# Kernel tuning notes

Hardware: AMD Instinct MI355X
Metric: run time of the kernel (lower is better)

Reference implementation:

```python
import jax, jax.numpy as jnp
import numpy as np

GROUPS = 8
EPS = 1e-5


def group_norm_dim1(x, gamma, beta):
    # Faithful to torch: GroupNorm treats dim 1 (height) as the channel axis.
    B, H, W, C = x.shape
    xg = x.reshape(B, GROUPS, H // GROUPS, W, C)
    mean = xg.mean(axis=(2, 3, 4), keepdims=True)
    var = xg.var(axis=(2, 3, 4), keepdims=True)
    xn = ((xg - mean) * jax.lax.rsqrt(var + EPS)).reshape(B, H, W, C)
    return xn * gamma[None, :, None, None] + beta[None, :, None, None]


def setup_inputs() -> dict:
    key = jax.random.key(0)
    ks = jax.random.split(key, 8)
    B, H, W, C = 4, 64, 64, 64  # height must equal units for GroupNorm to apply
    s = 1.0 / np.sqrt(C)
    return {
        "x": jax.random.normal(ks[0], (B, H, W, C), dtype=jnp.float32),
        "gamma": jnp.ones((C,), jnp.float32),
        "beta": jnp.zeros((C,), jnp.float32),
        "Wq": jax.random.normal(ks[1], (C, C), jnp.float32) * s,
        "bq": jnp.zeros((C,), jnp.float32),
        "Wk": jax.random.normal(ks[2], (C, C), jnp.float32) * s,
        "bk": jnp.zeros((C,), jnp.float32),
        "Wv": jax.random.normal(ks[3], (C, C), jnp.float32) * s,
        "bv": jnp.zeros((C,), jnp.float32),
        "Wo": jax.random.normal(ks[4], (C, C), jnp.float32) * s,
        "bo": jnp.zeros((C,), jnp.float32),
    }


def reference(x, gamma, beta, Wq, bq, Wk, bk, Wv, bv, Wo, bo):
    B, H, W, C = x.shape
    scale = C ** (-0.5)
    xn = group_norm_dim1(x, gamma, beta)
    q = xn @ Wq + bq
    k = xn @ Wk + bk
    v = xn @ Wv + bv
    # full spatial self-attention: scores [B, H, W, H*W]
    scores = jnp.einsum('bhwc,bijc->bhwij', q, k) * scale
    attn = jax.nn.softmax(scores.reshape(B, H, W, H * W), axis=-1)
    attn = attn.reshape(B, H, W, H, W)
    proj = jnp.einsum('bhwij,bijc->bhwc', attn, v)
    proj = proj @ Wo + bo
    return xn + proj
```

## Files before the change

### kernel.cpp

```cpp
#include <hip/hip_runtime.h>

typedef __bf16 bf16_t;
typedef bf16_t bf16x8 __attribute__((ext_vector_type(8)));
typedef bf16_t bf16x4 __attribute__((ext_vector_type(4)));
typedef float  f32x4  __attribute__((ext_vector_type(4)));

#define MFMA32(a, b, c) __builtin_amdgcn_mfma_f32_16x16x32_bf16(a, b, c, 0, 0, 0)

typedef __attribute__((address_space(3))) unsigned int       lds_u32;
typedef __attribute__((address_space(1))) const unsigned int glb_u32c;
#define DMA16(GP, LP) __builtin_amdgcn_global_load_lds((glb_u32c*)(const void*)(GP), \
                                                       (lds_u32*)(void*)(LP), 16, 0, 0)

__global__ __launch_bounds__(256) void gn1w_kernel(const float* __restrict__ x,
    float2* __restrict__ partials,
    const float* __restrict__ Wq, const float* __restrict__ Wk,
    const float* __restrict__ Wv, const float* __restrict__ Wo,
    bf16_t* __restrict__ Wt) {
  int blk = blockIdx.x, t = threadIdx.x;
  if (blk >= 256) {
    int idx = (blk - 256) * 256 + t;
    int wsel = idx >> 12, rem = idx & 4095;
    int c = rem >> 6, kk = rem & 63;
    const float* src = (wsel == 0) ? Wq : ((wsel == 1) ? Wk : ((wsel == 2) ? Wv : Wo));
    Wt[idx] = (bf16_t)src[kk * 64 + c];
    return;
  }
  const float4* x4 = (const float4*)x + (size_t)blk * 1024;
  float s = 0.f, sq = 0.f;
  #pragma unroll
  for (int u = 0; u < 4; ++u) {
    float4 v = x4[u * 256 + t];
    s  += v.x + v.y + v.z + v.w;
    sq += v.x * v.x + v.y * v.y + v.z * v.z + v.w * v.w;
  }
  for (int off = 32; off; off >>= 1) {
    s  += __shfl_down(s, off, 64);
    sq += __shfl_down(sq, off, 64);
  }
  __shared__ float2 ps[4];
  if ((t & 63) == 0) ps[t >> 6] = make_float2(s, sq);
  __syncthreads();
  if (t == 0) {
    float S = 0.f, Q = 0.f;
    #pragma unroll
    for (int i = 0; i < 4; ++i) { S += ps[i].x; Q += ps[i].y; }
    partials[blk] = make_float2(S, Q);
  }
}

__global__ __launch_bounds__(256) void gnqkv_kernel(
    const float* __restrict__ x, const float* __restrict__ gamma,
    const float* __restrict__ beta, const float2* __restrict__ parts,
    const bf16_t* __restrict__ Wt,
    const float* __restrict__ bq, const float* __restrict__ bk, const float* __restrict__ bv,
    bf16_t* __restrict__ xnb, bf16_t* __restrict__ qo, bf16_t* __restrict__ ko,
    bf16_t* __restrict__ vo) {
  __shared__ __align__(16) bf16_t xl[4096];
  int blk = blockIdx.x, t = threadIdx.x;
  int grp = blk >> 3;
  float S = 0.f, Q = 0.f;
  #pragma unroll
  for (int i = 0; i < 8; ++i) { float2 p = parts[grp * 8 + i]; S += p.x; Q += p.y; }
  float mean = S * (1.f / 32768.f);
  float rstd = rsqrtf(Q * (1.f / 32768.f) - mean * mean + 1e-5f);
  int h = blk & 63;
  float ga = gamma[h] * rstd;
  float be = beta[h] - mean * ga;
  {
    int r = t >> 2, col0 = (t & 3) * 16;
    const float4* x4 = (const float4*)(x + (size_t)blk * 4096 + r * 64 + col0);
    bf16x8 pk0, pk1;
    float4 v0 = x4[0], v1 = x4[1], v2 = x4[2], v3 = x4[3];
    pk0[0] = (bf16_t)(v0.x * ga + be); pk0[1] = (bf16_t)(v0.y * ga + be);
    pk0[2] = (bf16_t)(v0.z * ga + be); pk0[3] = (bf16_t)(v0.w * ga + be);
    pk0[4] = (bf16_t)(v1.x * ga + be); pk0[5] = (bf16_t)(v1.y * ga + be);
    pk0[6] = (bf16_t)(v1.z * ga + be); pk0[7] = (bf16_t)(v1.w * ga + be);
    pk1[0] = (bf16_t)(v2.x * ga + be); pk1[1] = (bf16_t)(v2.y * ga + be);
    pk1[2] = (bf16_t)(v2.z * ga + be); pk1[3] = (bf16_t)(v2.w * ga + be);
    pk1[4] = (bf16_t)(v3.x * ga + be); pk1[5] = (bf16_t)(v3.y * ga + be);
    pk1[6] = (bf16_t)(v3.z * ga + be); pk1[7] = (bf16_t)(v3.w * ga + be);
    *(bf16x8*)&xnb[(size_t)blk * 4096 + r * 64 + col0]     = pk0;
    *(bf16x8*)&xnb[(size_t)blk * 4096 + r * 64 + col0 + 8] = pk1;
    int sw = r & 7, j0 = (t & 3) * 2;
    *(bf16x8*)&xl[r * 64 + ((j0 ^ sw) << 3)]       = pk0;
    *(bf16x8*)&xl[r * 64 + (((j0 + 1) ^ sw) << 3)] = pk1;
  }
  __syncthreads();
  int w = t >> 6, lane = t & 63, quad = lane >> 4, l16 = lane & 15;
  int rl = w * 16 + l16, sw2 = rl & 7;
  bf16x8 a0 = *(const bf16x8*)&xl[rl * 64 + ((quad ^ sw2) << 3)];
  bf16x8 a1 = *(const bf16x8*)&xl[rl * 64 + (((quad + 4) ^ sw2) << 3)];
  int m0 = blk * 64 + w * 16;
  int bi = blk >> 6;
  int tile = blk & 63;
  size_t tbase = (size_t)bi * 262144 + (size_t)tile * 4096;
  f32x4 zero = {0.f, 0.f, 0.f, 0.f};
  const float QSCALE = 0.125f * 1.44269504088896340736f;
  #pragma unroll
  for (int outk = 0; outk < 3; ++outk) {
    const bf16_t* wt = Wt + outk * 4096;
    const float* bias = (outk == 0) ? bq : ((outk == 1) ? bk : bv);
    #pragma unroll
    for (int nt = 0; nt < 4; ++nt) {
      int col = nt * 16 + l16;
      bf16x8 b0 = *(const bf16x8*)&wt[col * 64 + quad * 8];
      bf16x8 b1 = *(const bf16x8*)&wt[col * 64 + 32 + quad * 8];
      f32x4 acc = MFMA32(a0, b0, zero);
      acc = MFMA32(a1, b1, acc);
      float bb = bias[col];
      if (outk == 0) {
        #pragma unroll
        for (int r = 0; r < 4; ++r) {
          int m = m0 + quad * 4 + r;
          qo[(size_t)m * 64 + col] = (bf16_t)((acc[r] + bb) * QSCALE);
        }
      } else if (outk == 1) {
        #pragma unroll
        for (int r = 0; r < 4; ++r) {
          int kk = (m0 & 63) + quad * 4 + r;
          ko[tbase + kk * 64 + ((((col >> 3) ^ (kk & 7)) << 3) | (col & 7))]
              = (bf16_t)(acc[r] + bb);
        }
      } else {
        bf16x4 pk;
        #pragma unroll
        for (int r = 0; r < 4; ++r) pk[r] = (bf16_t)(acc[r] + bb);
        int u = (w >> 1) * 8 + quad * 2 + (w & 1);
        *(bf16x4*)&vo[tbase + col * 64 + ((u ^ ((col & 7) << 1)) << 2)] = pk;
      }
    }
  }
}

__global__ __launch_bounds__(256, 2) void flash_kernel(
    const bf16_t* __restrict__ q, const bf16_t* __restrict__ k,
    const bf16_t* __restrict__ vp, bf16_t* __restrict__ Opb, float* __restrict__ ml) {
  __shared__ __align__(16) bf16_t Kb[2][8192];
  __shared__ __align__(16) bf16_t Vb[2][8192];
  int t = threadIdx.x;
  int w = t >> 6, lane = t & 63, quad = lane >> 4, l16 = lane & 15;
  int b = blockIdx.x, qb = blockIdx.y, sp = blockIdx.z;
  int q0 = qb * 128 + w * 32;

  bf16x8 qf[2][2];
  {
    const bf16_t* qp = q + ((size_t)b * 4096 + q0 + l16) * 64;
    #pragma unroll
    for (int qt = 0; qt < 2; ++qt)
      #pragma unroll
      for (int hh = 0; hh < 2; ++hh)
        qf[qt][hh] = *(const bf16x8*)&qp[qt * 1024 + hh * 32 + quad * 8];
  }
  f32x4 o[2][4];
  f32x4 zero = {0.f, 0.f, 0.f, 0.f};
  #pragma unroll
  for (int qt = 0; qt < 2; ++qt)
    #pragma unroll
    for (int ct = 0; ct < 4; ++ct) o[qt][ct] = zero;
  float rs[2] = {0.f, 0.f};

  const bf16_t* kimg = k  + (size_t)b * 262144 + (size_t)sp * 65536 + w * 2048 + lane * 8;
  const bf16_t* vimg = vp + (size_t)b * 262144 + (size_t)sp * 65536 + w * 2048 + lane * 8;

  #pragma unroll
  for (int i = 0; i < 4; ++i) {
    DMA16(kimg + i * 512, &Kb[0][w * 2048 + i * 512]);
    DMA16(vimg + i * 512, &Vb[0][w * 2048 + i * 512]);
  }
  __syncthreads();

  int swk = l16 & 7;
  int swv = (l16 & 7) << 1;

  for (int it = 0; it < 8; ++it) {
    int cur = it & 1;
    if (it < 7) {
      const bf16_t* kg = kimg + (it + 1) * 8192;
      const bf16_t* vg = vimg + (it + 1) * 8192;
      int nxt = cur ^ 1;
      #pragma unroll
      for (int i = 0; i < 4; ++i) {
        DMA16(kg + i * 512, &Kb[nxt][w * 2048 + i * 512]);
        DMA16(vg + i * 512, &Vb[nxt][w * 2048 + i * 512]);
      }
    }
    #pragma unroll
    for (int j = 0; j < 4; ++j) {
      const bf16_t* Kh = &Kb[cur][(j >> 1) * 4096];
      const bf16_t* Vh = &Vb[cur][(j >> 1) * 4096];
      int k2 = j & 1;
      int krow_a = ((k2 * 2) * 16 + l16) * 64;
      int krow_b = ((k2 * 2 + 1) * 16 + l16) * 64;
      bf16x8 kf0a = *(const bf16x8*)&Kh[krow_a + ((quad ^ swk) << 3)];
      bf16x8 kf1a = *(const bf16x8*)&Kh[krow_a + (((quad + 4) ^ swk) << 3)];
      bf16x8 kf0b = *(const bf16x8*)&Kh[krow_b + ((quad ^ swk) << 3)];
      bf16x8 kf1b = *(const bf16x8*)&Kh[krow_b + (((quad + 4) ^ swk) << 3)];
      int ub = k2 * 8 + quad * 2;
      bf16x8 va8[4];
      #pragma unroll
      for (int ct = 0; ct < 4; ++ct)
        va8[ct] = *(const bf16x8*)&Vh[(ct * 16 + l16) * 64 + ((ub ^ swv) << 2)];
      #pragma unroll
      for (int qt = 0; qt < 2; ++qt) {
        f32x4 sta = MFMA32(kf0a, qf[qt][0], zero);
        sta = MFMA32(kf1a, qf[qt][1], sta);
        f32x4 stb = MFMA32(kf0b, qf[qt][0], zero);
        stb = MFMA32(kf1b, qf[qt][1], stb);
        bf16x8 pb;
        float psum = 0.f;
        #pragma unroll
        for (int r = 0; r < 4; ++r) {
          float pa = __builtin_amdgcn_exp2f(sta[r]);
          float pc = __builtin_amdgcn_exp2f(stb[r]);
          psum += pa + pc;
          pb[r]     = (bf16_t)pa;
          pb[r + 4] = (bf16_t)pc;
        }
        rs[qt] += psum;
        #pragma unroll
        for (int ct = 0; ct < 4; ++ct)
          o[qt][ct] = MFMA32(va8[ct], pb, o[qt][ct]);
      }
    }
    __syncthreads();
  }

  #pragma unroll
  for (int qt = 0; qt < 2; ++qt) {
    rs[qt] += __shfl_xor(rs[qt], 16, 64);
    rs[qt] += __shfl_xor(rs[qt], 32, 64);
  }
  size_t rbase = (size_t)sp * 16384 + (size_t)b * 4096 + q0;
  #pragma unroll
  for (int qt = 0; qt < 2; ++qt)
    if (quad == 0) ml[rbase + qt * 16 + l16] = rs[qt];

  bf16_t* Ot = (bf16_t*)Kb;
  #pragma unroll
  for (int qt = 0; qt < 2; ++qt) {
    int R = w * 32 + qt * 16 + l16;
    int swz = l16 & 7;
    #pragma unroll
    for (int ct = 0; ct < 4; ++ct) {
      bf16x4 pk;
      #pragma unroll
      for (int r = 0; r < 4; ++r) pk[r] = (bf16_t)o[qt][ct][r];
      int ch = ct * 2 + (quad >> 1);
      *(bf16x4*)&Ot[R * 64 + ((ch ^ swz) << 3) + ((quad & 1) << 2)] = pk;
    }
  }
  __syncthreads();
  size_t obase = ((size_t)sp * 16384 + (size_t)b * 4096 + (size_t)qb * 128) * 64;
  #pragma unroll
  for (int j = 0; j < 4; ++j) {
    int R = j * 32 + (t >> 3);
    int ch = (t & 7) ^ ((t >> 3) & 7);
    bf16x8 vv = *(const bf16x8*)&Ot[R * 64 + (ch << 3)];
    *(bf16x8*)&Opb[obase + j * 2048 + t * 8] = vv;
  }
}

__global__ __launch_bounds__(256) void proj_kernel(
    const bf16_t* __restrict__ Opb, const float* __restrict__ ml,
    const bf16_t* __restrict__ Wt, const float* __restrict__ bo,
    const bf16_t* __restrict__ xnb, float* __restrict__ out) {
  int t = threadIdx.x, w = t >> 6, lane = t & 63, quad = lane >> 4, l16 = lane & 15;
  int r0 = blockIdx.x * 64 + w * 16;
  float acc0[8], acc1[8];
  #pragma unroll
  for (int e = 0; e < 8; ++e) { acc0[e] = 0.f; acc1[e] = 0.f; }
  float lsum = 0.f;
  #pragma unroll
  for (int s = 0; s < 4; ++s) {
    size_t rr = (size_t)s * 16384 + r0 + l16;
    bf16x8 f0 = *(const bf16x8*)&Opb[rr * 64 + quad * 8];
    bf16x8 f1 = *(const bf16x8*)&Opb[rr * 64 + 32 + quad * 8];
    #pragma unroll
    for (int e = 0; e < 8; ++e) { acc0[e] += (float)f0[e]; acc1[e] += (float)f1[e]; }
    lsum += ml[rr];
  }
  float linv = 1.f / lsum;
  bf16x8 a0, a1;
  #pragma unroll
  for (int e = 0; e < 8; ++e) {
    a0[e] = (bf16_t)(acc0[e] * linv);
    a1[e] = (bf16_t)(acc1[e] * linv);
  }
  f32x4 zero = {0.f, 0.f, 0.f, 0.f};
  const bf16_t* wt = Wt + 3 * 4096;
  #pragma unroll
  for (int nt = 0; nt < 4; ++nt) {
    int col = nt * 16 + l16;
    bf16x8 b0 = *(const bf16x8*)&wt[col * 64 + quad * 8];
    bf16x8 b1 = *(const bf16x8*)&wt[col * 64 + 32 + quad * 8];
    f32x4 acc = MFMA32(a0, b0, zero);
    acc = MFMA32(a1, b1, acc);
    float bb = bo[col];
    #pragma unroll
    for (int r = 0; r < 4; ++r) {
      size_t m = (size_t)r0 + quad * 4 + r;
      out[m * 64 + col] = acc[r] + bb + (float)xnb[m * 64 + col];
    }
  }
}

extern "C" void kernel_launch(void* const* d_in, const int* in_sizes, int n_in,
                              void* d_out, int out_size, void* d_ws, size_t ws_size,
                              hipStream_t stream) {
  const float* x     = (const float*)d_in[0];
  const float* gamma = (const float*)d_in[1];
  const float* beta  = (const float*)d_in[2];
  const float* Wq    = (const float*)d_in[3];
  const float* bq    = (const float*)d_in[4];
  const float* Wk    = (const float*)d_in[5];
  const float* bk    = (const float*)d_in[6];
  const float* Wv    = (const float*)d_in[7];
  const float* bv    = (const float*)d_in[8];
  const float* Wo    = (const float*)d_in[9];
  const float* bo    = (const float*)d_in[10];
  float* out = (float*)d_out;

  char* ws = (char*)d_ws;
  bf16_t* xnb   = (bf16_t*)(ws + 0);
  bf16_t* qbuf  = (bf16_t*)(ws + (2u  << 20));
  bf16_t* kbuf  = (bf16_t*)(ws + (4u  << 20));
  bf16_t* vbuf  = (bf16_t*)(ws + (6u  << 20));
  bf16_t* Opb   = (bf16_t*)(ws + (8u  << 20));
  float*  ml    = (float*)(ws + (16u << 20));
  float2* parts = (float2*)(ws + (17u << 20));
  bf16_t* Wt    = (bf16_t*)(ws + (17u << 20) + 4096);

  hipLaunchKernelGGL(gn1w_kernel,  dim3(320),       dim3(256), 0, stream, x, parts, Wq, Wk, Wv, Wo, Wt);
  hipLaunchKernelGGL(gnqkv_kernel, dim3(256),       dim3(256), 0, stream, x, gamma, beta, parts, Wt, bq, bk, bv, xnb, qbuf, kbuf, vbuf);
  hipLaunchKernelGGL(flash_kernel, dim3(4, 32, 4),  dim3(256), 0, stream, qbuf, kbuf, vbuf, Opb, ml);
  hipLaunchKernelGGL(proj_kernel,  dim3(256),       dim3(256), 0, stream, Opb, ml, Wt, bo, xnb, out);
}
```

Before: 118.2 us.

## Replace double-buffered K/V staging with a 4-deep ring using vmcnt waits

The flash kernel's K/V tiles are now staged into a 4-slot ring of half-size buffers, with three tiles in flight. Explicit s_waitcnt vmcnt counts plus a single barrier per tile replace the per-iteration __syncthreads and the blocking initial load. The aim is to hide global-to-LDS DMA latency behind the MFMA work. The trade-off is more barriers overall and reliance on hand-counted vmcnt values, which must match the exact number of outstanding loads.

Result: no change. 119.3 us (+0.9%).

```diff
diff --git a/kernel.cpp b/kernel.cpp
--- a/kernel.cpp
+++ b/kernel.cpp
@@ -136,8 +136,8 @@
 __global__ __launch_bounds__(256, 2) void flash_kernel(
     const bf16_t* __restrict__ q, const bf16_t* __restrict__ k,
     const bf16_t* __restrict__ vp, bf16_t* __restrict__ Opb, float* __restrict__ ml) {
-  __shared__ __align__(16) bf16_t Kb[2][8192];
-  __shared__ __align__(16) bf16_t Vb[2][8192];
+  __shared__ __align__(16) bf16_t Kb[4][4096];
+  __shared__ __align__(16) bf16_t Vb[4][4096];
   int t = threadIdx.x;
   int w = t >> 6, lane = t & 63, quad = lane >> 4, l16 = lane & 15;
   int b = blockIdx.x, qb = blockIdx.y, sp = blockIdx.z;
@@ -160,36 +160,36 @@
     for (int ct = 0; ct < 4; ++ct) o[qt][ct] = zero;
   float rs[2] = {0.f, 0.f};
 
-  const bf16_t* kimg = k  + (size_t)b * 262144 + (size_t)sp * 65536 + w * 2048 + lane * 8;
-  const bf16_t* vimg = vp + (size_t)b * 262144 + (size_t)sp * 65536 + w * 2048 + lane * 8;
-
-  #pragma unroll
-  for (int i = 0; i < 4; ++i) {
-    DMA16(kimg + i * 512, &Kb[0][w * 2048 + i * 512]);
-    DMA16(vimg + i * 512, &Vb[0][w * 2048 + i * 512]);
-  }
-  __syncthreads();
+  const bf16_t* kimg = k  + (size_t)b * 262144 + (size_t)sp * 65536 + w * 1024 + lane * 8;
+  const bf16_t* vimg = vp + (size_t)b * 262144 + (size_t)sp * 65536 + w * 1024 + lane * 8;
+
+  auto stage = [&](int img, int buf) {
+    const bf16_t* kg = kimg + img * 4096;
+    const bf16_t* vg = vimg + img * 4096;
+    DMA16(kg,       &Kb[buf][w * 1024]);
+    DMA16(kg + 512, &Kb[buf][w * 1024 + 512]);
+    DMA16(vg,       &Vb[buf][w * 1024]);
+    DMA16(vg + 512, &Vb[buf][w * 1024 + 512]);
+  };
+
+  stage(0, 0);
+  stage(1, 1);
+  stage(2, 2);
 
   int swk = l16 & 7;
   int swv = (l16 & 7) << 1;
 
-  for (int it = 0; it < 8; ++it) {
-    int cur = it & 1;
-    if (it < 7) {
-      const bf16_t* kg = kimg + (it + 1) * 8192;
-      const bf16_t* vg = vimg + (it + 1) * 8192;
-      int nxt = cur ^ 1;
-      #pragma unroll
-      for (int i = 0; i < 4; ++i) {
-        DMA16(kg + i * 512, &Kb[nxt][w * 2048 + i * 512]);
-        DMA16(vg + i * 512, &Vb[nxt][w * 2048 + i * 512]);
-      }
-    }
-    #pragma unroll
-    for (int j = 0; j < 4; ++j) {
-      const bf16_t* Kh = &Kb[cur][(j >> 1) * 4096];
-      const bf16_t* Vh = &Vb[cur][(j >> 1) * 4096];
-      int k2 = j & 1;
+  for (int img = 0; img < 16; ++img) {
+    if (img < 14)       asm volatile("s_waitcnt vmcnt(8)" ::: "memory");
+    else if (img == 14) asm volatile("s_waitcnt vmcnt(4)" ::: "memory");
+    else                asm volatile("s_waitcnt vmcnt(0)" ::: "memory");
+    __builtin_amdgcn_s_barrier();
+    __builtin_amdgcn_sched_barrier(0);
+    if (img + 3 < 16) stage(img + 3, (img + 3) & 3);
+    const bf16_t* Kh = Kb[img & 3];
+    const bf16_t* Vh = Vb[img & 3];
+    #pragma unroll
+    for (int k2 = 0; k2 < 2; ++k2) {
       int krow_a = ((k2 * 2) * 16 + l16) * 64;
       int krow_b = ((k2 * 2 + 1) * 16 + l16) * 64;
       bf16x8 kf0a = *(const bf16x8*)&Kh[krow_a + ((quad ^ swk) << 3)];
@@ -223,7 +223,6 @@
           o[qt][ct] = MFMA32(va8[ct], pb, o[qt][ct]);
       }
     }
-    __syncthreads();
   }
 
   #pragma unroll
```
